# Kernel tuning notes

Measured on AMD Instinct MI355X. Metric: run time of the kernel, lower is better.

Reference implementation:

```python
import jax, jax.numpy as jnp
import numpy as np

BAND_WIDTH = 0.5
EPS = 1e-5
NORM_EPS = 1e-12  # F.normalize eps


def setup_inputs() -> dict:
    key = jax.random.key(0)
    k1, k2 = jax.random.split(key)
    shape = (8, 512, 48, 48)  # N, C, H, W  (VGG conv4_4 features of a 384x384 image)
    return {
        "pred": jax.random.normal(k1, shape, dtype=jnp.float32),
        "target": jax.random.normal(k2, shape, dtype=jnp.float32),
    }


def reference(pred, target):
    N, C, H, W = pred.shape
    # center both by target channel-mean over (N, H, W)
    y_mu = jnp.mean(target, axis=(0, 2, 3), keepdims=True)
    x_c = pred - y_mu
    y_c = target - y_mu
    # L2-normalize along channel dim (F.normalize: divide by max(norm, eps))
    x_n = x_c / jnp.maximum(jnp.linalg.norm(x_c, axis=1, keepdims=True), NORM_EPS)
    y_n = y_c / jnp.maximum(jnp.linalg.norm(y_c, axis=1, keepdims=True), NORM_EPS)
    x_v = x_n.reshape(N, C, H * W)
    y_v = y_n.reshape(N, C, H * W)
    # pairwise cosine distance: [N, HW, HW]
    cosine_sim = jnp.einsum('ncp,ncq->npq', x_v, y_v)
    dist_raw = 1.0 - cosine_sim
    # relative distance: divide each row by its min over keys (dim=2)
    dist_min = jnp.min(dist_raw, axis=2, keepdims=True)
    dist_tilde = dist_raw / (dist_min + EPS)
    # similarity + row-normalize (softmax-like over dim=2)
    w = jnp.exp((1.0 - dist_tilde) / BAND_WIDTH)
    cx = w / jnp.sum(w, axis=2, keepdims=True)
    # max over query dim (dim=1), mean over key dim -> [N]
    cx = jnp.mean(jnp.max(cx, axis=1), axis=1)
    cx_loss = -jnp.log(cx + EPS)
    # reduction='mean', loss_weight=1.0
    return jnp.mean(cx_loss)
```

## Files before the change

### kernel.cpp

```cpp
#include <hip/hip_runtime.h>
#include <stdint.h>

#define NB 8
#define CC 512
#define PP 2304
#define EPSF 1e-5f
#define NPC 12
#define PCH 192

typedef short bf16x8 __attribute__((ext_vector_type(8)));
typedef float f32x4 __attribute__((ext_vector_type(4)));

typedef __attribute__((address_space(3))) uint8_t lds8_t;
typedef __attribute__((address_space(1))) const uint8_t g8_t;

__device__ __forceinline__ void async16(void* lds, const void* g) {
  __builtin_amdgcn_global_load_lds((g8_t*)g, (lds8_t*)lds, 16, 0, 0);
}

__device__ __forceinline__ float bf2f(uint32_t b16) {
  return __uint_as_float(b16 << 16);
}
__device__ __forceinline__ uint32_t f2bf(float f) {
  uint32_t u = __float_as_uint(f);
  return (u + 0x7fffu + ((u >> 16) & 1u)) >> 16;
}

template <int N>
__device__ __forceinline__ void vmwait() {
  if constexpr (N == 0) asm volatile("s_waitcnt vmcnt(0)" ::: "memory");
  else if constexpr (N == 4) asm volatile("s_waitcnt vmcnt(4)" ::: "memory");
  else if constexpr (N == 6) asm volatile("s_waitcnt vmcnt(6)" ::: "memory");
  else if constexpr (N == 8) asm volatile("s_waitcnt vmcnt(8)" ::: "memory");
}

__global__ __launch_bounds__(256) void k_chan_mean(const float* __restrict__ tgt,
                                                   float* __restrict__ mu) {
  const int c = blockIdx.x, t = threadIdx.x;
  float s = 0.f;
  for (int n = 0; n < NB; ++n) {
    const float* b = tgt + ((size_t)n * CC + c) * PP;
    for (int p = t; p < PP; p += 256) s += b[p];
  }
  for (int off = 32; off; off >>= 1) s += __shfl_down(s, off);
  __shared__ float red[4];
  if ((t & 63) == 0) red[t >> 6] = s;
  __syncthreads();
  if (t == 0) mu[c] = (red[0] + red[1] + red[2] + red[3]) * (1.0f / (NB * PP));
}

__global__ __launch_bounds__(256) void k_center_cast(
    const float* __restrict__ pred, const float* __restrict__ tgt,
    const float* __restrict__ mu,
    uint16_t* __restrict__ xt, uint16_t* __restrict__ yt,
    float* __restrict__ ssx, float* __restrict__ ssy) {
  __shared__ uint32_t lt[64][33];
  __shared__ float red[4][64];
  const int p0 = blockIdx.x * 64, c0 = blockIdx.y * 64, n = blockIdx.z;
  const int t = threadIdx.x, lp = t & 63, cb = t >> 6;
  for (int which = 0; which < 2; ++which) {
    const float* in = which ? tgt : pred;
    uint16_t* out = which ? yt : xt;
    float* ss = which ? ssy : ssx;
    float sq = 0.f;
    uint32_t packs[8];
#pragma unroll
    for (int i = 0; i < 16; ++i) {
      const int c = c0 + cb * 16 + i;
      float v = in[((size_t)n * CC + c) * PP + p0 + lp] - mu[c];
      sq += v * v;
      uint32_t b = f2bf(v);
      if (i & 1) packs[i >> 1] |= b << 16; else packs[i >> 1] = b;
    }
#pragma unroll
    for (int j = 0; j < 8; ++j) lt[lp][cb * 8 + j] = packs[j];
    red[cb][lp] = sq;
    __syncthreads();
    if (t < 64)
      atomicAdd(&ss[(size_t)n * PP + p0 + t],
                red[0][t] + red[1][t] + red[2][t] + red[3][t]);
    const int p = t >> 2, ch = t & 3;
    uint4 v0, v1;
    v0.x = lt[p][ch * 8 + 0]; v0.y = lt[p][ch * 8 + 1];
    v0.z = lt[p][ch * 8 + 2]; v0.w = lt[p][ch * 8 + 3];
    v1.x = lt[p][ch * 8 + 4]; v1.y = lt[p][ch * 8 + 5];
    v1.z = lt[p][ch * 8 + 6]; v1.w = lt[p][ch * 8 + 7];
    uint4* ob = (uint4*)(out + (((size_t)n * PP + p0 + p) * CC + c0 + ch * 16));
    ob[0] = v0; ob[1] = v1;
    __syncthreads();
  }
}


__device__ __forceinline__ void stage_half(uint16_t* reg, const uint16_t* g, int tid) {
  async16((char*)reg + tid * 16, g);
  async16((char*)reg + tid * 16 + 8192, g + 64 * CC);
}

template <int QM, int QN, bool LOADA, bool STG, int VM>
__device__ __forceinline__ void phase(const uint16_t (*R)[8192],
                                      uint16_t* sdst, const uint16_t* ssrc,
                                      int tid, int lane, int wr, int wcn,
                                      bf16x8 (&af)[4][2], f32x4 (&acc)[2][4][2][2]) {
  if (LOADA) {
#pragma unroll
    for (int i = 0; i < 4; ++i) {
      const int rh = wr * 64 + i * 16 + (lane & 15);
      const char* base = (const char*)R[QM] + rh * 128;
      const int sw = (rh & 7) << 4;
#pragma unroll
      for (int kk = 0; kk < 2; ++kk)
        af[i][kk] = *(const bf16x8*)(base + ((kk * 64 + (lane >> 4) * 16) ^ sw));
    }
  }
  bf16x8 bf[2][2];
#pragma unroll
  for (int j = 0; j < 2; ++j) {
    const int rh = wcn * 32 + j * 16 + (lane & 15);
    const char* base = (const char*)R[2 + QN] + rh * 128;
    const int sw = (rh & 7) << 4;
#pragma unroll
    for (int kk = 0; kk < 2; ++kk)
      bf[j][kk] = *(const bf16x8*)(base + ((kk * 64 + (lane >> 4) * 16) ^ sw));
  }
  if (STG) stage_half(sdst, ssrc, tid);
  __builtin_amdgcn_s_barrier();
  asm volatile("s_waitcnt lgkmcnt(0)" ::: "memory");
  __builtin_amdgcn_s_setprio(1);
#pragma unroll
  for (int i = 0; i < 4; ++i)
#pragma unroll
    for (int j = 0; j < 2; ++j)
#pragma unroll
      for (int kk = 0; kk < 2; ++kk)
        acc[QM][i][QN][j] = __builtin_amdgcn_mfma_f32_16x16x32_bf16(
            af[i][kk], bf[j][kk], acc[QM][i][QN][j], 0, 0, 0);
  __builtin_amdgcn_s_setprio(0);
  vmwait<VM>();
  __builtin_amdgcn_s_barrier();
}

__global__ __launch_bounds__(512, 2) void k_gemm(
    const uint16_t* __restrict__ xt, const uint16_t* __restrict__ yt,
    const float* __restrict__ ssx, const float* __restrict__ ssy,
    uint16_t* __restrict__ S) {
  __shared__ uint16_t lds[2][4][8192];
  int flat = blockIdx.x + 9 * blockIdx.y + 81 * blockIdx.z;
  flat = (flat & 7) * 81 + (flat >> 3);
  const int nb = flat / 81;
  const int rem = flat - nb * 81;
  const int m0 = (rem % 9) * 256, n0 = (rem / 9) * 256;
  const int tid = threadIdx.x, lane = tid & 63, wid = tid >> 6;
  const int wr = wid >> 2, wcn = wid & 3;
  const uint16_t* Ax = xt + (size_t)nb * PP * CC;
  const uint16_t* By = yt + (size_t)nb * PP * CC;
  const int lswz = (tid & 7) ^ ((tid >> 3) & 7);
  const uint16_t* gAb = Ax + (size_t)(m0 + (tid >> 3)) * CC + lswz * 8;
  const uint16_t* gBb = By + (size_t)(n0 + (tid >> 3)) * CC + lswz * 8;

  f32x4 acc[2][4][2][2];
#pragma unroll
  for (int a = 0; a < 2; ++a)
#pragma unroll
    for (int b = 0; b < 4; ++b)
#pragma unroll
      for (int c = 0; c < 2; ++c)
#pragma unroll
        for (int d = 0; d < 2; ++d) acc[a][b][c][d] = (f32x4){0.f, 0.f, 0.f, 0.f};

  stage_half(lds[0][0], gAb, tid);
  stage_half(lds[0][2], gBb, tid);
  stage_half(lds[0][1], gAb + 128 * CC, tid);
  stage_half(lds[0][3], gBb + 128 * CC, tid);
  stage_half(lds[1][0], gAb + 64, tid);
  stage_half(lds[1][2], gBb + 64, tid);
  vmwait<8>();
  __builtin_amdgcn_s_barrier();

  bf16x8 af[4][2];
  for (int kt = 0; kt < 6; ++kt) {
    const int cur = kt & 1;
    const uint16_t(*R)[8192] = lds[cur];
    uint16_t(*Wn)[8192] = lds[cur ^ 1];
    uint16_t(*Wc)[8192] = lds[cur];
    const int ko = (kt + 1) * 64;
    phase<0, 0, true, true, 6>(R, Wn[1], gAb + 128 * CC + ko, tid, lane, wr, wcn, af, acc);
    phase<0, 1, false, true, -1>(R, Wn[3], gBb + 128 * CC + ko, tid, lane, wr, wcn, af, acc);
    phase<1, 0, true, true, -1>(R, Wc[0], gAb + ko + 64, tid, lane, wr, wcn, af, acc);
    phase<1, 1, false, true, 8>(R, Wc[2], gBb + ko + 64, tid, lane, wr, wcn, af, acc);
  }
  {
    const uint16_t(*R)[8192] = lds[0];
    phase<0, 0, true, true, 6>(R, lds[1][1], gAb + 128 * CC + 7 * 64, tid, lane, wr, wcn, af, acc);
    phase<0, 1, false, true, -1>(R, lds[1][3], gBb + 128 * CC + 7 * 64, tid, lane, wr, wcn, af, acc);
    phase<1, 0, true, false, -1>(R, nullptr, nullptr, tid, lane, wr, wcn, af, acc);
    phase<1, 1, false, false, 4>(R, nullptr, nullptr, tid, lane, wr, wcn, af, acc);
  }
  {
    const uint16_t(*R)[8192] = lds[1];
    phase<0, 0, true, false, 0>(R, nullptr, nullptr, tid, lane, wr, wcn, af, acc);
    phase<0, 1, false, false, -1>(R, nullptr, nullptr, tid, lane, wr, wcn, af, acc);
    phase<1, 0, true, false, -1>(R, nullptr, nullptr, tid, lane, wr, wcn, af, acc);
    phase<1, 1, false, false, -1>(R, nullptr, nullptr, tid, lane, wr, wcn, af, acc);
  }

  const float* rsp = ssx + (size_t)nb * PP + m0;
  const float* csp = ssy + (size_t)nb * PP + n0;
  uint16_t* Sp = S + (size_t)nb * PP * PP;
  float cinv[2][2];
#pragma unroll
  for (int qn = 0; qn < 2; ++qn)
#pragma unroll
    for (int j = 0; j < 2; ++j)
      cinv[qn][j] =
          1.0f / fmaxf(sqrtf(csp[qn * 128 + wcn * 32 + j * 16 + (lane & 15)]), 1e-12f);
#pragma unroll
  for (int qm = 0; qm < 2; ++qm)
#pragma unroll
    for (int i = 0; i < 4; ++i)
#pragma unroll
      for (int r = 0; r < 4; ++r) {
        const int row = qm * 128 + wr * 64 + i * 16 + (lane >> 4) * 4 + r;
        const float ri = 1.0f / fmaxf(sqrtf(rsp[row]), 1e-12f);
        uint16_t* orow = Sp + (size_t)(m0 + row) * PP + n0;
#pragma unroll
        for (int qn = 0; qn < 2; ++qn)
#pragma unroll
          for (int j = 0; j < 2; ++j)
            orow[qn * 128 + wcn * 32 + j * 16 + (lane & 15)] =
                (uint16_t)f2bf(acc[qm][i][qn][j][r] * ri * cinv[qn][j]);
      }
}

__global__ __launch_bounds__(256) void k_rowstats(const uint16_t* __restrict__ S,
                                                  float* __restrict__ dmin,
                                                  float* __restrict__ rsum) {
  const int row = blockIdx.x;
  const uint2* Sp = (const uint2*)(S + (size_t)row * PP);
  __shared__ __align__(16) float cosr[PP];
  __shared__ float reda[4], redb[4];
  const int t = threadIdx.x;
  float mx = -2.f;
  for (int i = t; i < PP / 4; i += 256) {
    uint2 u = Sp[i];
    float a = bf2f(u.x & 0xffffu), b = bf2f(u.x >> 16);
    float c = bf2f(u.y & 0xffffu), d = bf2f(u.y >> 16);
    *(float4*)&cosr[4 * i] = make_float4(a, b, c, d);
    mx = fmaxf(fmaxf(mx, fmaxf(a, b)), fmaxf(c, d));
  }
  for (int off = 32; off; off >>= 1) mx = fmaxf(mx, __shfl_down(mx, off));
  if ((t & 63) == 0) reda[t >> 6] = mx;
  __syncthreads();
  mx = fmaxf(fmaxf(reda[0], reda[1]), fmaxf(reda[2], reda[3]));
  const float dm = 1.0f - mx;
  const float sc = 2.0f / (dm + EPSF);
  float s = 0.f;
  for (int i = t; i < PP; i += 256) s += __expf((cosr[i] - mx + EPSF) * sc);
  for (int off = 32; off; off >>= 1) s += __shfl_down(s, off);
  if ((t & 63) == 0) redb[t >> 6] = s;
  __syncthreads();
  if (t == 0) { dmin[row] = dm; rsum[row] = redb[0] + redb[1] + redb[2] + redb[3]; }
}

__global__ __launch_bounds__(256) void k_colmax_part(const uint16_t* __restrict__ S,
                                                     const float* __restrict__ dmin,
                                                     const float* __restrict__ rsum,
                                                     float* __restrict__ pcm) {
  const int n = blockIdx.y, pc = blockIdx.z, t = threadIdx.x;
  const int q2 = blockIdx.x * 512 + 2 * t;
  __shared__ float lmx[PCH], lsc[PCH], lri[PCH];
  const float* dmn = dmin + (size_t)n * PP + pc * PCH;
  const float* rsn = rsum + (size_t)n * PP + pc * PCH;
  for (int i = t; i < PCH; i += 256) {
    float dm = dmn[i];
    lmx[i] = 1.0f - dm - EPSF;
    lsc[i] = 2.0f / (dm + EPSF);
    lri[i] = 1.0f / rsn[i];
  }
  __syncthreads();
  if (q2 >= PP) return;
  const uint32_t* Sn =
      (const uint32_t*)(S + (size_t)n * PP * PP + (size_t)pc * PCH * PP + q2);
  float b0 = 0.f, b1 = 0.f;
#pragma unroll 8
  for (int p = 0; p < PCH; ++p) {
    uint32_t u = Sn[(size_t)p * (PP / 2)];
    float mxv = lmx[p], scv = lsc[p], riv = lri[p];
    b0 = fmaxf(b0, __expf((bf2f(u & 0xffffu) - mxv) * scv) * riv);
    b1 = fmaxf(b1, __expf((bf2f(u >> 16) - mxv) * scv) * riv);
  }
  float* o = pcm + ((size_t)n * NPC + pc) * PP + q2;
  o[0] = b0; o[1] = b1;
}

__global__ __launch_bounds__(256) void k_colmax_fin(const float* __restrict__ pcm,
                                                    float* __restrict__ cxacc) {
  const int n = blockIdx.y, t = threadIdx.x;
  const int q = blockIdx.x * 256 + t;
  float best = 0.f;
#pragma unroll
  for (int c = 0; c < NPC; ++c) best = fmaxf(best, pcm[((size_t)n * NPC + c) * PP + q]);
  float s = best;
  for (int off = 32; off; off >>= 1) s += __shfl_down(s, off);
  __shared__ float red[4];
  if ((t & 63) == 0) red[t >> 6] = s;
  __syncthreads();
  if (t == 0) atomicAdd(&cxacc[n], red[0] + red[1] + red[2] + red[3]);
}

__global__ void k_final(const float* __restrict__ cxacc, float* __restrict__ out) {
  if (threadIdx.x == 0 && blockIdx.x == 0) {
    float s = 0.f;
    for (int n = 0; n < NB; ++n) {
      float cx = cxacc[n] * (1.0f / PP);
      s += -logf(cx + EPSF);
    }
    out[0] = s * (1.0f / NB);
  }
}

extern "C" void kernel_launch(void* const* d_in, const int* in_sizes, int n_in,
                              void* d_out, int out_size, void* d_ws, size_t ws_size,
                              hipStream_t stream) {
  const float* pred = (const float*)d_in[0];
  const float* tgt  = (const float*)d_in[1];
  float* W = (float*)d_ws;
  float* mu   = W + 0;
  float* ssx  = W + 1024;
  float* ssy  = W + 19456;
  float* cx   = W + 37888;
  float* dmin = W + 75264;
  float* rsum = W + 93696;
  uint16_t* xt = (uint16_t*)(W + 223744);
  uint16_t* yt = xt + (size_t)NB * PP * CC;
  uint16_t* S  = yt + (size_t)NB * PP * CC;
  float* pcm = (float*)xt;

  hipMemsetAsync(W + 1024, 0, (36872) * sizeof(float), stream);

  k_chan_mean<<<dim3(CC), dim3(256), 0, stream>>>(tgt, mu);
  k_center_cast<<<dim3(PP / 64, CC / 64, NB), dim3(256), 0, stream>>>(
      pred, tgt, mu, xt, yt, ssx, ssy);
  k_gemm<<<dim3(9, 9, NB), dim3(512), 0, stream>>>(xt, yt, ssx, ssy, S);
  k_rowstats<<<dim3(NB * PP), dim3(256), 0, stream>>>(S, dmin, rsum);
  k_colmax_part<<<dim3((PP + 511) / 512, NB, NPC), dim3(256), 0, stream>>>(
      S, dmin, rsum, pcm);
  k_colmax_fin<<<dim3(PP / 256, NB), dim3(256), 0, stream>>>(pcm, cx);
  k_final<<<1, 64, 0, stream>>>(cx, (float*)d_out);
}
```

Measured before the change: 159.7 us.

## Fold centering into GEMM epilogue, fuse rowstats with colmax, restage GEMM loads

The separate channel-mean pass is gone. The mean is now accumulated with atomics inside the cast kernel, which stores uncentered bf16. The centering correction is applied algebraically in the GEMM epilogue through per-row mu·x dot products from a new small GEMV kernel, with matching norm adjustments. The row-stats and column-max kernels are merged into one kernel that computes row max and sum for a 24-row chunk and then updates column maxima with integer atomicMax. This removes one full read of S and the partial buffer. The GEMM phase order and B-fragment reuse are also changed, along with how many tiles are prefetched per phase. The main risk is precision: centering after rounding to bf16 and subtracting large terms in fp32 can lose accuracy.

```diff
diff --git a/kernel.cpp b/kernel.cpp
--- a/kernel.cpp
+++ b/kernel.cpp
@@ -5,8 +5,6 @@
 #define CC 512
 #define PP 2304
 #define EPSF 1e-5f
-#define NPC 12
-#define PCH 192
 
 typedef short bf16x8 __attribute__((ext_vector_type(8)));
 typedef float f32x4 __attribute__((ext_vector_type(4)));
@@ -18,9 +16,8 @@
   __builtin_amdgcn_global_load_lds((g8_t*)g, (lds8_t*)lds, 16, 0, 0);
 }
 
-__device__ __forceinline__ float bf2f(uint32_t b16) {
-  return __uint_as_float(b16 << 16);
-}
+__device__ __forceinline__ float bf2lo(uint32_t u) { return __uint_as_float(u << 16); }
+__device__ __forceinline__ float bf2hi(uint32_t u) { return __uint_as_float(u & 0xffff0000u); }
 __device__ __forceinline__ uint32_t f2bf(float f) {
   uint32_t u = __float_as_uint(f);
   return (u + 0x7fffu + ((u >> 16) & 1u)) >> 16;
@@ -29,31 +26,15 @@
 template <int N>
 __device__ __forceinline__ void vmwait() {
   if constexpr (N == 0) asm volatile("s_waitcnt vmcnt(0)" ::: "memory");
+  else if constexpr (N == 2) asm volatile("s_waitcnt vmcnt(2)" ::: "memory");
   else if constexpr (N == 4) asm volatile("s_waitcnt vmcnt(4)" ::: "memory");
   else if constexpr (N == 6) asm volatile("s_waitcnt vmcnt(6)" ::: "memory");
-  else if constexpr (N == 8) asm volatile("s_waitcnt vmcnt(8)" ::: "memory");
-}
-
-__global__ __launch_bounds__(256) void k_chan_mean(const float* __restrict__ tgt,
-                                                   float* __restrict__ mu) {
-  const int c = blockIdx.x, t = threadIdx.x;
-  float s = 0.f;
-  for (int n = 0; n < NB; ++n) {
-    const float* b = tgt + ((size_t)n * CC + c) * PP;
-    for (int p = t; p < PP; p += 256) s += b[p];
-  }
-  for (int off = 32; off; off >>= 1) s += __shfl_down(s, off);
-  __shared__ float red[4];
-  if ((t & 63) == 0) red[t >> 6] = s;
-  __syncthreads();
-  if (t == 0) mu[c] = (red[0] + red[1] + red[2] + red[3]) * (1.0f / (NB * PP));
-}
-
-__global__ __launch_bounds__(256) void k_center_cast(
+}
+
+__global__ __launch_bounds__(256) void k_cast(
     const float* __restrict__ pred, const float* __restrict__ tgt,
-    const float* __restrict__ mu,
     uint16_t* __restrict__ xt, uint16_t* __restrict__ yt,
-    float* __restrict__ ssx, float* __restrict__ ssy) {
+    float* __restrict__ ssx, float* __restrict__ ssy, float* __restrict__ musum) {
   __shared__ uint32_t lt[64][33];
   __shared__ float red[4][64];
   const int p0 = blockIdx.x * 64, c0 = blockIdx.y * 64, n = blockIdx.z;
@@ -63,14 +44,25 @@
     uint16_t* out = which ? yt : xt;
     float* ss = which ? ssy : ssx;
     float sq = 0.f;
+    float tmp[16];
     uint32_t packs[8];
 #pragma unroll
     for (int i = 0; i < 16; ++i) {
       const int c = c0 + cb * 16 + i;
-      float v = in[((size_t)n * CC + c) * PP + p0 + lp] - mu[c];
+      float v = in[((size_t)n * CC + c) * PP + p0 + lp];
+      tmp[i] = v;
       sq += v * v;
       uint32_t b = f2bf(v);
       if (i & 1) packs[i >> 1] |= b << 16; else packs[i >> 1] = b;
+    }
+    if (which) {
+#pragma unroll
+      for (int i = 0; i < 16; ++i) {
+        float s = tmp[i];
+#pragma unroll
+        for (int d = 1; d < 64; d <<= 1) s += __shfl_xor(s, d);
+        if (lp == 0) atomicAdd(&musum[c0 + cb * 16 + i], s);
+      }
     }
 #pragma unroll
     for (int j = 0; j < 8; ++j) lt[lp][cb * 8 + j] = packs[j];
@@ -91,18 +83,55 @@
   }
 }
 
-
-__device__ __forceinline__ void stage_half(uint16_t* reg, const uint16_t* g, int tid) {
-  async16((char*)reg + tid * 16, g);
-  async16((char*)reg + tid * 16 + 8192, g + 64 * CC);
-}
-
-template <int QM, int QN, bool LOADA, bool STG, int VM>
+__global__ __launch_bounds__(256) void k_gemv(
+    const float* __restrict__ musum,
+    const uint16_t* __restrict__ xt, const uint16_t* __restrict__ yt,
+    float* __restrict__ mvx, float* __restrict__ mvy) {
+  const uint16_t* T = blockIdx.y ? yt : xt;
+  float* mv = blockIdx.y ? mvy : mvx;
+  __shared__ float mu_l[512];
+  __shared__ float m2red[4];
+  const int t = threadIdx.x, w = t >> 6, lane = t & 63;
+  const float scale = 1.0f / (NB * PP);
+  float m2p = 0.f;
+  for (int i = t; i < 512; i += 256) {
+    float m = musum[i] * scale;
+    mu_l[i] = m;
+    m2p += m * m;
+  }
+#pragma unroll
+  for (int d = 1; d < 64; d <<= 1) m2p += __shfl_xor(m2p, d);
+  if (lane == 0) m2red[w] = m2p;
+  __syncthreads();
+  const float mu2h = 0.5f * (m2red[0] + m2red[1] + m2red[2] + m2red[3]);
+  for (int it = 0; it < 16; ++it) {
+    const int r = blockIdx.x * 64 + w * 16 + it;
+    uint4 u = *(const uint4*)(T + (size_t)r * CC + lane * 8);
+    float s = 0.f;
+    const float* m = &mu_l[lane * 8];
+    s += bf2lo(u.x) * m[0] + bf2hi(u.x) * m[1];
+    s += bf2lo(u.y) * m[2] + bf2hi(u.y) * m[3];
+    s += bf2lo(u.z) * m[4] + bf2hi(u.z) * m[5];
+    s += bf2lo(u.w) * m[6] + bf2hi(u.w) * m[7];
+#pragma unroll
+    for (int d = 1; d < 64; d <<= 1) s += __shfl_xor(s, d);
+    if (lane == 0) mv[r] = s - mu2h;
+  }
+}
+
+__device__ __forceinline__ void stage_half(uint16_t* dst, const uint16_t* g, int tid) {
+  async16((char*)dst + tid * 16, g);
+  async16((char*)dst + tid * 16 + 8192, g + 64 * CC);
+}
+
+template <int QM, int QN, bool LA, bool LB, int VM>
 __device__ __forceinline__ void phase(const uint16_t (*R)[8192],
-                                      uint16_t* sdst, const uint16_t* ssrc,
+                                      uint16_t* d1, const uint16_t* s1,
+                                      uint16_t* d2, const uint16_t* s2,
                                       int tid, int lane, int wr, int wcn,
-                                      bf16x8 (&af)[4][2], f32x4 (&acc)[2][4][2][2]) {
-  if (LOADA) {
+                                      bf16x8 (&af)[4][2], bf16x8 (&bfv)[2][2],
+                                      f32x4 (&acc)[2][4][2][2]) {
+  if (LA) {
 #pragma unroll
     for (int i = 0; i < 4; ++i) {
       const int rh = wr * 64 + i * 16 + (lane & 15);
@@ -113,17 +142,19 @@
         af[i][kk] = *(const bf16x8*)(base + ((kk * 64 + (lane >> 4) * 16) ^ sw));
     }
   }
-  bf16x8 bf[2][2];
-#pragma unroll
-  for (int j = 0; j < 2; ++j) {
-    const int rh = wcn * 32 + j * 16 + (lane & 15);
-    const char* base = (const char*)R[2 + QN] + rh * 128;
-    const int sw = (rh & 7) << 4;
-#pragma unroll
-    for (int kk = 0; kk < 2; ++kk)
-      bf[j][kk] = *(const bf16x8*)(base + ((kk * 64 + (lane >> 4) * 16) ^ sw));
-  }
-  if (STG) stage_half(sdst, ssrc, tid);
+  if (LB) {
+#pragma unroll
+    for (int j = 0; j < 2; ++j) {
+      const int rh = wcn * 32 + j * 16 + (lane & 15);
+      const char* base = (const char*)R[2 + QN] + rh * 128;
+      const int sw = (rh & 7) << 4;
+#pragma unroll
+      for (int kk = 0; kk < 2; ++kk)
+        bfv[j][kk] = *(const bf16x8*)(base + ((kk * 64 + (lane >> 4) * 16) ^ sw));
+    }
+  }
+  if (d1) stage_half(d1, s1, tid);
+  if (d2) stage_half(d2, s2, tid);
   __builtin_amdgcn_s_barrier();
   asm volatile("s_waitcnt lgkmcnt(0)" ::: "memory");
   __builtin_amdgcn_s_setprio(1);
@@ -134,7 +165,7 @@
 #pragma unroll
       for (int kk = 0; kk < 2; ++kk)
         acc[QM][i][QN][j] = __builtin_amdgcn_mfma_f32_16x16x32_bf16(
-            af[i][kk], bf[j][kk], acc[QM][i][QN][j], 0, 0, 0);
+            af[i][kk], bfv[j][kk], acc[QM][i][QN][j], 0, 0, 0);
   __builtin_amdgcn_s_setprio(0);
   vmwait<VM>();
   __builtin_amdgcn_s_barrier();
@@ -143,6 +174,7 @@
 __global__ __launch_bounds__(512, 2) void k_gemm(
     const uint16_t* __restrict__ xt, const uint16_t* __restrict__ yt,
     const float* __restrict__ ssx, const float* __restrict__ ssy,
+    const float* __restrict__ mvx, const float* __restrict__ mvy,
     uint16_t* __restrict__ S) {
   __shared__ uint16_t lds[2][4][8192];
   int flat = blockIdx.x + 9 * blockIdx.y + 81 * blockIdx.z;
@@ -173,47 +205,62 @@
   stage_half(lds[0][1], gAb + 128 * CC, tid);
   stage_half(lds[0][3], gBb + 128 * CC, tid);
   stage_half(lds[1][0], gAb + 64, tid);
-  stage_half(lds[1][2], gBb + 64, tid);
-  vmwait<8>();
+  vmwait<6>();
   __builtin_amdgcn_s_barrier();
 
-  bf16x8 af[4][2];
+  bf16x8 af[4][2], bfv[2][2];
   for (int kt = 0; kt < 6; ++kt) {
-    const int cur = kt & 1;
-    const uint16_t(*R)[8192] = lds[cur];
-    uint16_t(*Wn)[8192] = lds[cur ^ 1];
-    uint16_t(*Wc)[8192] = lds[cur];
-    const int ko = (kt + 1) * 64;
-    phase<0, 0, true, true, 6>(R, Wn[1], gAb + 128 * CC + ko, tid, lane, wr, wcn, af, acc);
-    phase<0, 1, false, true, -1>(R, Wn[3], gBb + 128 * CC + ko, tid, lane, wr, wcn, af, acc);
-    phase<1, 0, true, true, -1>(R, Wc[0], gAb + ko + 64, tid, lane, wr, wcn, af, acc);
-    phase<1, 1, false, true, 8>(R, Wc[2], gBb + ko + 64, tid, lane, wr, wcn, af, acc);
+    const uint16_t(*R)[8192] = lds[kt & 1];
+    uint16_t(*Wn)[8192] = lds[(kt & 1) ^ 1];
+    uint16_t(*Wc)[8192] = lds[kt & 1];
+    const int ko1 = (kt + 1) * 64, ko2 = (kt + 2) * 64;
+    phase<0, 0, true, true, 6>(R, Wn[1], gAb + 128 * CC + ko1, Wn[2], gBb + ko1,
+                               tid, lane, wr, wcn, af, bfv, acc);
+    phase<0, 1, false, true, -1>(R, Wn[3], gBb + 128 * CC + ko1, nullptr, nullptr,
+                                 tid, lane, wr, wcn, af, bfv, acc);
+    phase<1, 1, true, false, -1>(R, Wc[0], gAb + ko2, nullptr, nullptr,
+                                 tid, lane, wr, wcn, af, bfv, acc);
+    phase<1, 0, false, true, 4>(R, nullptr, nullptr, nullptr, nullptr,
+                                tid, lane, wr, wcn, af, bfv, acc);
   }
   {
     const uint16_t(*R)[8192] = lds[0];
-    phase<0, 0, true, true, 6>(R, lds[1][1], gAb + 128 * CC + 7 * 64, tid, lane, wr, wcn, af, acc);
-    phase<0, 1, false, true, -1>(R, lds[1][3], gBb + 128 * CC + 7 * 64, tid, lane, wr, wcn, af, acc);
-    phase<1, 0, true, false, -1>(R, nullptr, nullptr, tid, lane, wr, wcn, af, acc);
-    phase<1, 1, false, false, 4>(R, nullptr, nullptr, tid, lane, wr, wcn, af, acc);
+    phase<0, 0, true, true, 6>(R, lds[1][1], gAb + 128 * CC + 7 * 64,
+                               lds[1][2], gBb + 7 * 64, tid, lane, wr, wcn, af, bfv, acc);
+    phase<0, 1, false, true, -1>(R, lds[1][3], gBb + 128 * CC + 7 * 64, nullptr, nullptr,
+                                 tid, lane, wr, wcn, af, bfv, acc);
+    phase<1, 1, true, false, -1>(R, nullptr, nullptr, nullptr, nullptr,
+                                 tid, lane, wr, wcn, af, bfv, acc);
+    phase<1, 0, false, true, 2>(R, nullptr, nullptr, nullptr, nullptr,
+                                tid, lane, wr, wcn, af, bfv, acc);
   }
   {
     const uint16_t(*R)[8192] = lds[1];
-    phase<0, 0, true, false, 0>(R, nullptr, nullptr, tid, lane, wr, wcn, af, acc);
-    phase<0, 1, false, false, -1>(R, nullptr, nullptr, tid, lane, wr, wcn, af, acc);
-    phase<1, 0, true, false, -1>(R, nullptr, nullptr, tid, lane, wr, wcn, af, acc);
-    phase<1, 1, false, false, -1>(R, nullptr, nullptr, tid, lane, wr, wcn, af, acc);
+    phase<0, 0, true, true, 0>(R, nullptr, nullptr, nullptr, nullptr,
+                               tid, lane, wr, wcn, af, bfv, acc);
+    phase<0, 1, false, true, -1>(R, nullptr, nullptr, nullptr, nullptr,
+                                 tid, lane, wr, wcn, af, bfv, acc);
+    phase<1, 1, true, false, -1>(R, nullptr, nullptr, nullptr, nullptr,
+                                 tid, lane, wr, wcn, af, bfv, acc);
+    phase<1, 0, false, true, -1>(R, nullptr, nullptr, nullptr, nullptr,
+                                 tid, lane, wr, wcn, af, bfv, acc);
   }
 
   const float* rsp = ssx + (size_t)nb * PP + m0;
   const float* csp = ssy + (size_t)nb * PP + n0;
+  const float* mvr = mvx + (size_t)nb * PP + m0;
+  const float* mvc = mvy + (size_t)nb * PP + n0;
   uint16_t* Sp = S + (size_t)nb * PP * PP;
-  float cinv[2][2];
+  float cinv[2][2], cmv[2][2];
 #pragma unroll
   for (int qn = 0; qn < 2; ++qn)
 #pragma unroll
-    for (int j = 0; j < 2; ++j)
-      cinv[qn][j] =
-          1.0f / fmaxf(sqrtf(csp[qn * 128 + wcn * 32 + j * 16 + (lane & 15)]), 1e-12f);
+    for (int j = 0; j < 2; ++j) {
+      const int col = qn * 128 + wcn * 32 + j * 16 + (lane & 15);
+      const float m = mvc[col];
+      cmv[qn][j] = m;
+      cinv[qn][j] = 1.0f / fmaxf(sqrtf(csp[col] - 2.0f * m), 1e-12f);
+    }
 #pragma unroll
   for (int qm = 0; qm < 2; ++qm)
 #pragma unroll
@@ -221,91 +268,78 @@
 #pragma unroll
       for (int r = 0; r < 4; ++r) {
         const int row = qm * 128 + wr * 64 + i * 16 + (lane >> 4) * 4 + r;
-        const float ri = 1.0f / fmaxf(sqrtf(rsp[row]), 1e-12f);
+        const float mr = mvr[row];
+        const float rinv = 1.0f / fmaxf(sqrtf(rsp[row] - 2.0f * mr), 1e-12f);
         uint16_t* orow = Sp + (size_t)(m0 + row) * PP + n0;
 #pragma unroll
         for (int qn = 0; qn < 2; ++qn)
 #pragma unroll
           for (int j = 0; j < 2; ++j)
-            orow[qn * 128 + wcn * 32 + j * 16 + (lane & 15)] =
-                (uint16_t)f2bf(acc[qm][i][qn][j][r] * ri * cinv[qn][j]);
+            orow[qn * 128 + wcn * 32 + j * 16 + (lane & 15)] = (uint16_t)f2bf(
+                (acc[qm][i][qn][j][r] - mr - cmv[qn][j]) * rinv * cinv[qn][j]);
       }
 }
 
-__global__ __launch_bounds__(256) void k_rowstats(const uint16_t* __restrict__ S,
-                                                  float* __restrict__ dmin,
-                                                  float* __restrict__ rsum) {
-  const int row = blockIdx.x;
-  const uint2* Sp = (const uint2*)(S + (size_t)row * PP);
-  __shared__ __align__(16) float cosr[PP];
-  __shared__ float reda[4], redb[4];
-  const int t = threadIdx.x;
-  float mx = -2.f;
-  for (int i = t; i < PP / 4; i += 256) {
-    uint2 u = Sp[i];
-    float a = bf2f(u.x & 0xffffu), b = bf2f(u.x >> 16);
-    float c = bf2f(u.y & 0xffffu), d = bf2f(u.y >> 16);
-    *(float4*)&cosr[4 * i] = make_float4(a, b, c, d);
-    mx = fmaxf(fmaxf(mx, fmaxf(a, b)), fmaxf(c, d));
-  }
-  for (int off = 32; off; off >>= 1) mx = fmaxf(mx, __shfl_down(mx, off));
-  if ((t & 63) == 0) reda[t >> 6] = mx;
+__global__ __launch_bounds__(256) void k_rowcol(const uint16_t* __restrict__ S,
+                                                int* __restrict__ cxcol) {
+  const int pc = blockIdx.x, n = blockIdx.y;
+  __shared__ float lsc[24], lb[24], lri[24];
+  const int t = threadIdx.x, w = t >> 6, lane = t & 63;
+  const size_t Sn = (size_t)n * PP * PP;
+  for (int it = 0; it < 6; ++it) {
+    const int r = w * 6 + it;
+    const uint2* rp = (const uint2*)(S + Sn + (size_t)(pc * 24 + r) * PP);
+    uint2 u[9];
+#pragma unroll
+    for (int k = 0; k < 9; ++k) u[k] = rp[lane + k * 64];
+    float v[36];
+#pragma unroll
+    for (int k = 0; k < 9; ++k) {
+      v[4 * k + 0] = bf2lo(u[k].x);
+      v[4 * k + 1] = bf2hi(u[k].x);
+      v[4 * k + 2] = bf2lo(u[k].y);
+      v[4 * k + 3] = bf2hi(u[k].y);
+    }
+    float mx = v[0];
+#pragma unroll
+    for (int k = 1; k < 36; ++k) mx = fmaxf(mx, v[k]);
+#pragma unroll
+    for (int d = 1; d < 64; d <<= 1) mx = fmaxf(mx, __shfl_xor(mx, d));
+    const float sc = 2.0f / (1.0f - mx + EPSF);
+    const float b = (EPSF - mx) * sc;
+    float s = 0.f;
+#pragma unroll
+    for (int k = 0; k < 36; ++k) s += __expf(fmaf(v[k], sc, b));
+#pragma unroll
+    for (int d = 1; d < 64; d <<= 1) s += __shfl_xor(s, d);
+    if (lane == 0) { lsc[r] = sc; lb[r] = b; lri[r] = 1.0f / s; }
+  }
   __syncthreads();
-  mx = fmaxf(fmaxf(reda[0], reda[1]), fmaxf(reda[2], reda[3]));
-  const float dm = 1.0f - mx;
-  const float sc = 2.0f / (dm + EPSF);
+  const uint32_t* Sc = (const uint32_t*)(S + Sn + (size_t)(pc * 24) * PP);
+  for (int pi = t; pi < PP / 2; pi += 256) {
+    float b0 = 0.f, b1 = 0.f;
+#pragma unroll
+    for (int r = 0; r < 24; ++r) {
+      const uint32_t u = Sc[(size_t)r * (PP / 2) + pi];
+      b0 = fmaxf(b0, __expf(fmaf(bf2lo(u), lsc[r], lb[r])) * lri[r]);
+      b1 = fmaxf(b1, __expf(fmaf(bf2hi(u), lsc[r], lb[r])) * lri[r]);
+    }
+    atomicMax(&cxcol[n * PP + 2 * pi], __float_as_int(b0));
+    atomicMax(&cxcol[n * PP + 2 * pi + 1], __float_as_int(b1));
+  }
+}
+
+__global__ __launch_bounds__(256) void k_colfin(const int* __restrict__ cxcol,
+                                                float* __restrict__ cxacc) {
+  const int n = blockIdx.x, t = threadIdx.x;
   float s = 0.f;
-  for (int i = t; i < PP; i += 256) s += __expf((cosr[i] - mx + EPSF) * sc);
-  for (int off = 32; off; off >>= 1) s += __shfl_down(s, off);
-  if ((t & 63) == 0) redb[t >> 6] = s;
-  __syncthreads();
-  if (t == 0) { dmin[row] = dm; rsum[row] = redb[0] + redb[1] + redb[2] + redb[3]; }
-}
-
-__global__ __launch_bounds__(256) void k_colmax_part(const uint16_t* __restrict__ S,
-                                                     const float* __restrict__ dmin,
-                                                     const float* __restrict__ rsum,
-                                                     float* __restrict__ pcm) {
-  const int n = blockIdx.y, pc = blockIdx.z, t = threadIdx.x;
-  const int q2 = blockIdx.x * 512 + 2 * t;
-  __shared__ float lmx[PCH], lsc[PCH], lri[PCH];
-  const float* dmn = dmin + (size_t)n * PP + pc * PCH;
-  const float* rsn = rsum + (size_t)n * PP + pc * PCH;
-  for (int i = t; i < PCH; i += 256) {
-    float dm = dmn[i];
-    lmx[i] = 1.0f - dm - EPSF;
-    lsc[i] = 2.0f / (dm + EPSF);
-    lri[i] = 1.0f / rsn[i];
-  }
-  __syncthreads();
-  if (q2 >= PP) return;
-  const uint32_t* Sn =
-      (const uint32_t*)(S + (size_t)n * PP * PP + (size_t)pc * PCH * PP + q2);
-  float b0 = 0.f, b1 = 0.f;
-#pragma unroll 8
-  for (int p = 0; p < PCH; ++p) {
-    uint32_t u = Sn[(size_t)p * (PP / 2)];
-    float mxv = lmx[p], scv = lsc[p], riv = lri[p];
-    b0 = fmaxf(b0, __expf((bf2f(u & 0xffffu) - mxv) * scv) * riv);
-    b1 = fmaxf(b1, __expf((bf2f(u >> 16) - mxv) * scv) * riv);
-  }
-  float* o = pcm + ((size_t)n * NPC + pc) * PP + q2;
-  o[0] = b0; o[1] = b1;
-}
-
-__global__ __launch_bounds__(256) void k_colmax_fin(const float* __restrict__ pcm,
-                                                    float* __restrict__ cxacc) {
-  const int n = blockIdx.y, t = threadIdx.x;
-  const int q = blockIdx.x * 256 + t;
-  float best = 0.f;
-#pragma unroll
-  for (int c = 0; c < NPC; ++c) best = fmaxf(best, pcm[((size_t)n * NPC + c) * PP + q]);
-  float s = best;
-  for (int off = 32; off; off >>= 1) s += __shfl_down(s, off);
+  for (int q = t; q < PP; q += 256) s += __int_as_float(cxcol[n * PP + q]);
+#pragma unroll
+  for (int d = 1; d < 64; d <<= 1) s += __shfl_xor(s, d);
   __shared__ float red[4];
   if ((t & 63) == 0) red[t >> 6] = s;
   __syncthreads();
-  if (t == 0) atomicAdd(&cxacc[n], red[0] + red[1] + red[2] + red[3]);
+  if (t == 0) cxacc[n] = red[0] + red[1] + red[2] + red[3];
 }
 
 __global__ void k_final(const float* __restrict__ cxacc, float* __restrict__ out) {
@@ -325,26 +359,24 @@
   const float* pred = (const float*)d_in[0];
   const float* tgt  = (const float*)d_in[1];
   float* W = (float*)d_ws;
-  float* mu   = W + 0;
-  float* ssx  = W + 1024;
-  float* ssy  = W + 19456;
-  float* cx   = W + 37888;
-  float* dmin = W + 75264;
-  float* rsum = W + 93696;
-  uint16_t* xt = (uint16_t*)(W + 223744);
+  float* musum = W + 0;
+  float* ssx   = W + 512;
+  float* ssy   = W + 18944;
+  int*   cxcol = (int*)(W + 37376);
+  float* cxacc = W + 55808;
+  float* mvx   = W + 56320;
+  float* mvy   = W + 74752;
+  uint16_t* xt = (uint16_t*)(W + 93440);
   uint16_t* yt = xt + (size_t)NB * PP * CC;
   uint16_t* S  = yt + (size_t)NB * PP * CC;
-  float* pcm = (float*)xt;
-
-  hipMemsetAsync(W + 1024, 0, (36872) * sizeof(float), stream);
-
-  k_chan_mean<<<dim3(CC), dim3(256), 0, stream>>>(tgt, mu);
-  k_center_cast<<<dim3(PP / 64, CC / 64, NB), dim3(256), 0, stream>>>(
-      pred, tgt, mu, xt, yt, ssx, ssy);
-  k_gemm<<<dim3(9, 9, NB), dim3(512), 0, stream>>>(xt, yt, ssx, ssy, S);
-  k_rowstats<<<dim3(NB * PP), dim3(256), 0, stream>>>(S, dmin, rsum);
-  k_colmax_part<<<dim3((PP + 511) / 512, NB, NPC), dim3(256), 0, stream>>>(
-      S, dmin, rsum, pcm);
-  k_colmax_fin<<<dim3(PP / 256, NB), dim3(256), 0, stream>>>(pcm, cx);
-  k_final<<<1, 64, 0, stream>>>(cx, (float*)d_out);
-}
+
+  hipMemsetAsync(W, 0, 55808 * sizeof(float), stream);
+
+  k_cast<<<dim3(PP / 64, CC / 64, NB), dim3(256), 0, stream>>>(
+      pred, tgt, xt, yt, ssx, ssy, musum);
+  k_gemv<<<dim3(288, 2), dim3(256), 0, stream>>>(musum, xt, yt, mvx, mvy);
+  k_gemm<<<dim3(9, 9, NB), dim3(512), 0, stream>>>(xt, yt, ssx, ssy, mvx, mvy, S);
+  k_rowcol<<<dim3(96, NB), dim3(256), 0, stream>>>(S, cxcol);
+  k_colfin<<<dim3(NB), dim3(256), 0, stream>>>(cxcol, cxacc);
+  k_final<<<1, 64, 0, stream>>>(cxacc, (float*)d_out);
+}
```

After: 256.8 us. +60.8%, slower.
